# Performance work log

Measured on AMD Instinct MI355X. Metric: run time of the kernel, lower is better.

Reference implementation:

```python
import jax, jax.numpy as jnp
import numpy as np

B_, N_, D_ = 8, 1024, 64
H_, DH_ = 4, 16
DI_, DS_, DTR_ = 128, 64, 4
MAXP = 512


def _ln(x, w, b, eps=1e-5):
    m = jnp.mean(x, -1, keepdims=True)
    v = jnp.mean((x - m) ** 2, -1, keepdims=True)
    return (x - m) * jax.lax.rsqrt(v + eps) * w + b


def _attn(x, drop_mask, Wq, Wkv, Wo, bo, rel_emb):
    b, n, d = x.shape
    scale = DH_ ** -0.5
    q = (x @ Wq).reshape(b, n, H_, DH_).transpose(0, 2, 1, 3)
    kv = x @ Wkv
    k = kv[..., :d].reshape(b, n, H_, DH_).transpose(0, 2, 1, 3)
    v = kv[..., d:].reshape(b, n, H_, DH_).transpose(0, 2, 1, 3)
    dots = jnp.einsum('bhid,bhjd->bhij', q, k) * scale
    seq = jnp.arange(n)
    dist = jnp.clip(seq[:, None] - seq[None, :], -MAXP, MAXP) + MAXP
    rpe = rel_emb[dist]  # (n, n, DH_)
    dots = dots + jnp.einsum('bhid,ijd->bhij', q, rpe) * scale
    # stochastic key drop: Bernoulli(0.3) positions get -1e12
    dots = dots + drop_mask.astype(dots.dtype) * (-1e12)
    attn = jax.nn.softmax(dots, axis=-1)
    out = jnp.einsum('bhij,bhjd->bhid', attn, v)
    out = out.transpose(0, 2, 1, 3).reshape(b, n, H_ * DH_)
    return out @ Wo + bo


def _mamba(x, W_in, conv_w, conv_b, W_xproj, W_dt, b_dt, A_log, Dm, W_out):
    b, n, _ = x.shape
    xz = x @ W_in                      # (b, n, 2*DI_)
    u, z = xz[..., :DI_], xz[..., DI_:]
    uc = u.transpose(0, 2, 1)          # (b, DI_, n)
    uc = jax.lax.conv_general_dilated(
        uc, conv_w[:, None, :], (1,), ((3, 0),),
        feature_group_count=DI_, dimension_numbers=('NCH', 'OIH', 'NCH'))
    uc = uc + conv_b[None, :, None]
    u = jax.nn.silu(uc).transpose(0, 2, 1)  # (b, n, DI_)
    xdb = u @ W_xproj                  # (b, n, DTR_+2*DS_)
    dt = jax.nn.softplus(xdb[..., :DTR_] @ W_dt + b_dt)  # (b, n, DI_)
    Bm = xdb[..., DTR_:DTR_ + DS_]
    Cm = xdb[..., DTR_ + DS_:]
    A = -jnp.exp(A_log)                # (DI_, DS_)

    def step(h, inp):
        dt_t, B_t, C_t, u_t = inp      # (b,DI_),(b,DS_),(b,DS_),(b,DI_)
        dA = jnp.exp(dt_t[..., None] * A)
        h = h * dA + (dt_t * u_t)[..., None] * B_t[:, None, :]
        y = jnp.einsum('bds,bs->bd', h, C_t)
        return h, y

    h0 = jnp.zeros((b, DI_, DS_), x.dtype)
    xs = (dt.transpose(1, 0, 2), Bm.transpose(1, 0, 2),
          Cm.transpose(1, 0, 2), u.transpose(1, 0, 2))
    _, ys = jax.lax.scan(step, h0, xs)
    y = ys.transpose(1, 0, 2) + u * Dm
    y = y * jax.nn.silu(z)
    return y @ W_out


def _rmsgn(x, gamma, eps=1e-5, groups=4):
    shp = x.shape
    dpg = shp[-1] // groups
    xg = x.reshape(shp[:-1] + (groups, dpg))
    rms = jnp.sqrt(jnp.sum(xg * xg, -1, keepdims=True)) * (dpg ** -0.5)
    return (xg / (rms + eps)).reshape(shp) * gamma


def _ff1(x, c1_w, c1_b, d1_w, d1_b):
    # SwiGLUConvDeconv1d(64, 256, kernel=4, shift=1); x: (b, s2, 64)
    s2 = x.shape[1]
    xc = x.transpose(0, 2, 1)
    xc = jnp.pad(xc, ((0, 0), (0, 0), (3, 3)))
    xc = jax.lax.conv_general_dilated(
        xc, c1_w, (1,), 'VALID', dimension_numbers=('NCH', 'OIH', 'NCH'))
    xc = xc + c1_b[None, :, None]
    gate = jax.nn.silu(xc[:, 256:, :])
    xc = xc[:, :256, :] * gate
    # ConvTranspose1d stride 1 == conv with flipped kernel, full padding
    w = jnp.flip(d1_w, -1).transpose(1, 0, 2)  # (64, 256, 4)
    xc = jax.lax.conv_general_dilated(
        xc, w, (1,), ((3, 3),), dimension_numbers=('NCH', 'OIH', 'NCH'))
    xc = xc + d1_b[None, :, None]
    out = xc.transpose(0, 2, 1)
    return out[:, 3:3 + s2, :]


def _forward(x, drop_mask, ln1_w, ln1_b, Wq, Wkv, Wo, bo, rel_emb,
             ln2_w, ln2_b, W_in, conv_w, conv_b, W_xproj, W_dt, b_dt,
             A_log, Dm, W_out, gamma, c1_w, c1_b, d1_w, d1_b, ln3_w, ln3_b):
    xt = _ln(x, ln1_w, ln1_b)
    xt = _attn(xt, drop_mask, Wq, Wkv, Wo, bo, rel_emb) + x
    x = x + xt  # dropout p=0 -> identity (faithful to original residual math)
    xt = _ln(x, ln2_w, ln2_b)
    m = _mamba(xt, W_in, conv_w, conv_b, W_xproj, W_dt, b_dt, A_log, Dm, W_out)
    m = jnp.where(m >= 0, m, 0.01 * m)  # leaky_relu
    m = _rmsgn(m, gamma)
    m = m + 0.5 * _ff1(m, c1_w, c1_b, d1_w, d1_b)
    x = x + m
    return _ln(x, ln3_w, ln3_b)


def setup_inputs() -> dict:
    ks = jax.random.split(jax.random.key(0), 16)
    g = lambda i, shp, s: jax.random.normal(ks[i], shp, dtype=jnp.float32) * s
    A_log = jnp.log(jnp.tile(jnp.arange(1, DS_ + 1, dtype=jnp.float32)[None, :], (DI_, 1)))
    return {
        'x': jax.random.normal(ks[0], (B_, N_, D_), dtype=jnp.float32),
        'drop_mask': jax.random.bernoulli(ks[1], 0.3, (B_, H_, N_, N_)),
        'ln1_w': jnp.ones((D_,), jnp.float32), 'ln1_b': jnp.zeros((D_,), jnp.float32),
        'Wq': g(2, (D_, D_), 0.1), 'Wkv': g(3, (D_, 2 * D_), 0.1),
        'Wo': g(4, (D_, D_), 0.1), 'bo': jnp.zeros((D_,), jnp.float32),
        'rel_emb': g(5, (2 * MAXP + 1, DH_), 0.02),
        'ln2_w': jnp.ones((D_,), jnp.float32), 'ln2_b': jnp.zeros((D_,), jnp.float32),
        'W_in': g(6, (D_, 2 * DI_), 0.1),
        'conv_w': g(7, (DI_, 4), 0.2), 'conv_b': jnp.zeros((DI_,), jnp.float32),
        'W_xproj': g(8, (DI_, DTR_ + 2 * DS_), 0.1),
        'W_dt': g(9, (DTR_, DI_), 0.1), 'b_dt': jnp.zeros((DI_,), jnp.float32),
        'A_log': A_log, 'Dm': jnp.ones((DI_,), jnp.float32),
        'W_out': g(10, (DI_, D_), 0.1),
        'gamma': jnp.ones((D_,), jnp.float32),
        'c1_w': g(11, (512, 64, 4), 0.1), 'c1_b': jnp.zeros((512,), jnp.float32),
        'd1_w': g(12, (256, 64, 4), 0.1), 'd1_b': jnp.zeros((64,), jnp.float32),
        'ln3_w': jnp.ones((D_,), jnp.float32), 'ln3_b': jnp.zeros((D_,), jnp.float32),
    }


def reference(x, drop_mask, ln1_w, ln1_b, Wq, Wkv, Wo, bo, rel_emb,
              ln2_w, ln2_b, W_in, conv_w, conv_b, W_xproj, W_dt, b_dt,
              A_log, Dm, W_out, gamma, c1_w, c1_b, d1_w, d1_b, ln3_w, ln3_b):
    return _forward(x, drop_mask, ln1_w, ln1_b, Wq, Wkv, Wo, bo, rel_emb,
                    ln2_w, ln2_b, W_in, conv_w, conv_b, W_xproj, W_dt, b_dt,
                    A_log, Dm, W_out, gamma, c1_w, c1_b, d1_w, d1_b, ln3_w, ln3_b)
```

## Files before the change

### kernel.cpp

```cpp
#include <hip/hip_runtime.h>
#include <hip/hip_fp16.h>
#include <math.h>


__device__ __forceinline__ float wsum64(float v){
#pragma unroll
  for(int m=32;m>0;m>>=1) v += __shfl_xor(v, m, 64);
  return v;
}
__device__ __forceinline__ float wmax64(float v){
#pragma unroll
  for(int m=32;m>0;m>>=1) v = fmaxf(v, __shfl_xor(v, m, 64));
  return v;
}
__device__ __forceinline__ float silu_f(float x){ return x / (1.f + __expf(-x)); }
__device__ __forceinline__ float rfl_f(float x){
  return __int_as_float(__builtin_amdgcn_readfirstlane(__float_as_int(x)));
}

__global__ __launch_bounds__(256) void k_ln1_qkv(
    const float* __restrict__ x, const float* __restrict__ w1, const float* __restrict__ b1,
    const float* __restrict__ Wq, const float* __restrict__ Wkv,
    const float* __restrict__ rel, const float* __restrict__ c1w,
    const int* __restrict__ dmask,
    float* __restrict__ qb, float2* __restrict__ kvT,
    float* __restrict__ relT, float* __restrict__ c1wT,
    unsigned long long* __restrict__ mask64, unsigned* __restrict__ KmaxSq){
  int tid = threadIdx.x;
  int bi = blockIdx.x >> 1;
  if (blockIdx.x & 1){
    size_t base = (size_t)bi * 16384;
    const int4* dp4 = (const int4*)(dmask + base);
    unsigned long long* mp = mask64 + (base >> 6);
    int lane = tid & 63, wv = tid >> 6;
    int li = (lane & 15) * 4;
#pragma unroll 1
    for(int p=0; p<4; ++p){
      int4 v0 = dp4[p*1024 + tid*4 + 0];
      int4 v1 = dp4[p*1024 + tid*4 + 1];
      int4 v2 = dp4[p*1024 + tid*4 + 2];
      int4 v3 = dp4[p*1024 + tid*4 + 3];
      unsigned m = 0;
      m |= (v0.x!=0) ? 1u<<0  : 0u;  m |= (v0.y!=0) ? 1u<<1  : 0u;
      m |= (v0.z!=0) ? 1u<<2  : 0u;  m |= (v0.w!=0) ? 1u<<3  : 0u;
      m |= (v1.x!=0) ? 1u<<4  : 0u;  m |= (v1.y!=0) ? 1u<<5  : 0u;
      m |= (v1.z!=0) ? 1u<<6  : 0u;  m |= (v1.w!=0) ? 1u<<7  : 0u;
      m |= (v2.x!=0) ? 1u<<8  : 0u;  m |= (v2.y!=0) ? 1u<<9  : 0u;
      m |= (v2.z!=0) ? 1u<<10 : 0u;  m |= (v2.w!=0) ? 1u<<11 : 0u;
      m |= (v3.x!=0) ? 1u<<12 : 0u;  m |= (v3.y!=0) ? 1u<<13 : 0u;
      m |= (v3.z!=0) ? 1u<<14 : 0u;  m |= (v3.w!=0) ? 1u<<15 : 0u;
      unsigned s0 = __shfl(m, li+0, 64);
      unsigned s1 = __shfl(m, li+1, 64);
      unsigned s2 = __shfl(m, li+2, 64);
      unsigned s3 = __shfl(m, li+3, 64);
      if (lane < 16){
        unsigned long long word = (unsigned long long)s0
          | ((unsigned long long)s1 << 16)
          | ((unsigned long long)s2 << 32)
          | ((unsigned long long)s3 << 48);
        mp[p*64 + wv*16 + lane] = word;
      }
    }
    return;
  }
  int lane = tid & 63, warp = tid >> 6;
  int token = bi*4 + warp;
  __shared__ float xt[4][64];
  float xv = x[(size_t)token*64 + lane];
  float mean = wsum64(xv) * 0.015625f;
  float dlt = xv - mean;
  float var = wsum64(dlt*dlt) * 0.015625f;
  float xn = dlt * rsqrtf(var + 1e-5f) * w1[lane] + b1[lane];
  xt[warp][lane] = xn;
  __syncthreads();
  float aq=0.f, ak=0.f, av=0.f;
#pragma unroll 4
  for(int dd=0; dd<64; ++dd){
    float xd = xt[warp][dd];
    aq += xd * Wq[dd*64 + lane];
    ak += xd * Wkv[dd*128 + lane];
    av += xd * Wkv[dd*128 + 64 + lane];
  }
  int b = token >> 10, i = token & 1023;
  int h = lane >> 4, dh = lane & 15;
  size_t o  = (((size_t)(b*4 + h))*1024 + i)*16 + dh;
  size_t oT = (((size_t)(b*4 + h))*16 + dh)*1024 + i;
  qb[o]=aq;
  kvT[oT] = make_float2(ak, av);

  float kk = ak*ak;
  kk += __shfl_xor(kk, 1, 64);
  kk += __shfl_xor(kk, 2, 64);
  kk += __shfl_xor(kk, 4, 64);
  kk += __shfl_xor(kk, 8, 64);
  if (dh == 0) atomicMax(KmaxSq + (b*4 + h), __float_as_uint(kk));

  if (bi < 65){
    int idx = bi*256 + tid;
    if (idx < 16*1025){
      int c = idx / 1025;
      int d = idx - c*1025;
      relT[idx] = rel[d*16 + c];
    }
  } else if (bi < 577){
    int idx = (bi-65)*256 + tid;
    int row = idx >> 9;
    int ii  = idx & 511;
    c1wT[idx] = c1w[(size_t)ii*256 + row];
  }
}

__global__ __launch_bounds__(256, 2) void k_attn(
    const float* __restrict__ qb, const float2* __restrict__ kvT,
    const unsigned long long* __restrict__ mask64, const float* __restrict__ relT,
    const unsigned* __restrict__ KmaxSq, float* __restrict__ attn_raw){
  int tid = threadIdx.x;
  int lane = tid & 63;
  int wvu  = __builtin_amdgcn_readfirstlane(tid >> 6);
  int wg   = blockIdx.x;
  int xcd  = wg & 7;
  int slot = wg >> 3;
  int bh   = xcd*4 + (slot >> 6);
  int i0   = (slot & 63) * 16;
  int b = bh >> 2, h = bh & 3;
  int R0 = wvu*4, R1 = R0+1, R2 = R0+2, R3 = R0+3;

  __shared__ __align__(16) __half Gc[16][1040];
  __shared__ __align__(16) float4 kXV[2][64][9];
  __shared__ float qs[16][16];
  __shared__ float G0s[16], G1024s[16];
  __shared__ float gmS[16];
  __shared__ float Ms[16];
  __shared__ float sums[16];

  {
    int r = tid >> 4, c = tid & 15;
    qs[r][c] = qb[((size_t)bh*1024 + i0 + r)*16 + c] * 0.25f;
  }
  __syncthreads();

  float q0[16], q1[16], q2[16], q3[16];
#pragma unroll
  for(int c=0;c<16;++c){
    q0[c]=rfl_f(qs[R0][c]); q1[c]=rfl_f(qs[R1][c]);
    q2[c]=rfl_f(qs[R2][c]); q3[c]=rfl_f(qs[R3][c]);
  }

  const float2* kvb = kvT + (size_t)bh*16*1024;
  int jj = tid & 63, cg = tid >> 6;
  float2 st[4];
#define LOADREGS(CH) do{ int _j0=(CH)*64;                                   \
    _Pragma("unroll")                                                       \
    for(int i_=0;i_<4;++i_) st[i_]=kvb[(cg*4+i_)*1024 + _j0 + jj]; }while(0)
#define WRITEB(NB) do{                                                      \
    kXV[NB][jj][cg]  =make_float4(st[0].x,st[1].x,st[2].x,st[3].x);         \
    kXV[NB][jj][4+cg]=make_float4(st[0].y,st[1].y,st[2].y,st[3].y); }while(0)
#define LBAR() do{                                                          \
    asm volatile("s_waitcnt lgkmcnt(0)" ::: "memory");                      \
    __builtin_amdgcn_s_barrier();                                           \
    asm volatile("" ::: "memory"); }while(0)

  LOADREGS(0);

#pragma unroll 1
  for(int bb=0; bb<17; ++bb){
    int d = lane + 64*bb;
    if (d <= 1024){
      float rl[16];
#pragma unroll
      for(int c=0;c<16;++c) rl[c] = relT[c*1025 + d];
      float g0=0.f, g1=0.f, g2=0.f, g3=0.f;
#pragma unroll
      for(int c=0;c<16;++c){
        float rc = rl[c];
        g0 += q0[c]*rc; g1 += q1[c]*rc; g2 += q2[c]*rc; g3 += q3[c]*rc;
      }
      if (d == 0){ G0s[R0]=g0; G0s[R1]=g1; G0s[R2]=g2; G0s[R3]=g3; }
      else if (d == 1024){ G1024s[R0]=g0; G1024s[R1]=g1; G1024s[R2]=g2; G1024s[R3]=g3; }
      else {
        int j0r = i0 + 512 - d + R0;
        if (j0r+0 >= 0 && j0r+0 < 1024) Gc[R0][j0r+0] = __float2half_rn(g0);
        if (j0r+1 >= 0 && j0r+1 < 1024) Gc[R1][j0r+1] = __float2half_rn(g1);
        if (j0r+2 >= 0 && j0r+2 < 1024) Gc[R2][j0r+2] = __float2half_rn(g2);
        if (j0r+3 >= 0 && j0r+3 < 1024) Gc[R3][j0r+3] = __float2half_rn(g3);
      }
    }
  }
  __syncthreads();
  {
    const unsigned long long* mrow = mask64 + ((size_t)bh*1024 + i0)*16;
#pragma unroll 1
    for(int r=0;r<16;++r){
      float g0 = G0s[r], g1 = G1024s[r];
      int lo = i0 + r - 512;
      int hi = i0 + r + 512;
#pragma unroll
      for(int p=0;p<4;++p){
        int j = tid + 256*p;
        unsigned long long w = mrow[r*16 + (j>>6)];
        float g;
        if (j >= hi) g = g0;
        else if (j <= lo) g = g1;
        else g = __half2float(Gc[r][j]);
        if ((w >> (j & 63)) & 1ULL) g = -60000.f;
        Gc[r][j] = __float2half_rn(g);
      }
    }
  }
  __syncthreads();
  {
    int r = tid >> 4, l4 = tid & 15;
    float gm = -3.0e38f;
#pragma unroll
    for(int k=0;k<64;++k) gm = fmaxf(gm, __half2float(Gc[r][l4 + 16*k]));
#pragma unroll
    for(int m=1;m<16;m<<=1) gm = fmaxf(gm, __shfl_xor(gm, m, 64));
    if (l4 == 0) gmS[r] = gm;
  }
  __syncthreads();
  if (tid < 16){
    float qn = 0.f;
#pragma unroll
    for(int c=0;c<16;++c) qn += qs[tid][c]*qs[tid][c];
    float km = sqrtf(__uint_as_float(KmaxSq[bh]));
    Ms[tid] = gmS[tid] + sqrtf(qn)*km;
  }
  __syncthreads();

  float M0 = rfl_f(Ms[R0]), M1 = rfl_f(Ms[R1]);
  float M2 = rfl_f(Ms[R2]), M3 = rfl_f(Ms[R3]);

  float s0=0.f, s1=0.f, s2=0.f, s3=0.f;
  float a0[16], a1[16], a2[16], a3[16];
#pragma unroll
  for(int c=0;c<16;++c){ a0[c]=0.f; a1[c]=0.f; a2[c]=0.f; a3[c]=0.f; }

  WRITEB(0);
  LOADREGS(1);
  LBAR();
  int cur = 0;

#pragma unroll 1
  for(int ch=0; ch<16; ++ch){
    int j = ch*64 + lane;
    float sv0 = __half2float(Gc[R0][j]), sv1 = __half2float(Gc[R1][j]);
    float sv2 = __half2float(Gc[R2][j]), sv3 = __half2float(Gc[R3][j]);
#pragma unroll
    for(int c4=0;c4<4;++c4){
      float4 kx = kXV[cur][lane][c4];
      sv0 += q0[4*c4+0]*kx.x + q0[4*c4+1]*kx.y + q0[4*c4+2]*kx.z + q0[4*c4+3]*kx.w;
      sv1 += q1[4*c4+0]*kx.x + q1[4*c4+1]*kx.y + q1[4*c4+2]*kx.z + q1[4*c4+3]*kx.w;
      sv2 += q2[4*c4+0]*kx.x + q2[4*c4+1]*kx.y + q2[4*c4+2]*kx.z + q2[4*c4+3]*kx.w;
      sv3 += q3[4*c4+0]*kx.x + q3[4*c4+1]*kx.y + q3[4*c4+2]*kx.z + q3[4*c4+3]*kx.w;
    }
    float p0 = __expf(sv0 - M0), p1 = __expf(sv1 - M1);
    float p2 = __expf(sv2 - M2), p3 = __expf(sv3 - M3);
    s0 += p0; s1 += p1; s2 += p2; s3 += p3;
#pragma unroll
    for(int c4=0;c4<4;++c4){
      float4 vy = kXV[cur][lane][4+c4];
      a0[4*c4+0] += p0*vy.x; a0[4*c4+1] += p0*vy.y; a0[4*c4+2] += p0*vy.z; a0[4*c4+3] += p0*vy.w;
      a1[4*c4+0] += p1*vy.x; a1[4*c4+1] += p1*vy.y; a1[4*c4+2] += p1*vy.z; a1[4*c4+3] += p1*vy.w;
      a2[4*c4+0] += p2*vy.x; a2[4*c4+1] += p2*vy.y; a2[4*c4+2] += p2*vy.z; a2[4*c4+3] += p2*vy.w;
      a3[4*c4+0] += p3*vy.x; a3[4*c4+1] += p3*vy.y; a3[4*c4+2] += p3*vy.z; a3[4*c4+3] += p3*vy.w;
    }
    if (ch < 15){
      WRITEB(cur^1);
      if (ch < 14) LOADREGS(ch+2);
    }
    LBAR();
    cur ^= 1;
  }
#undef LOADREGS
#undef WRITEB
#undef LBAR

  s0 = wsum64(s0); s1 = wsum64(s1); s2 = wsum64(s2); s3 = wsum64(s3);
#pragma unroll
  for(int c=0;c<16;++c){
    float x0 = a0[c]; x0 += __shfl_xor(x0,32,64); x0 += __shfl_xor(x0,16,64); a0[c] = x0;
    float x1 = a1[c]; x1 += __shfl_xor(x1,32,64); x1 += __shfl_xor(x1,16,64); a1[c] = x1;
    float x2 = a2[c]; x2 += __shfl_xor(x2,32,64); x2 += __shfl_xor(x2,16,64); a2[c] = x2;
    float x3 = a3[c]; x3 += __shfl_xor(x3,32,64); x3 += __shfl_xor(x3,16,64); a3[c] = x3;
  }
  __syncthreads();
  float* red = (float*)&Gc[0][0];
  if (lane < 16){
#pragma unroll
    for(int c=0;c<16;++c){
      red[R0*272 + lane*17 + c] = a0[c];
      red[R1*272 + lane*17 + c] = a1[c];
      red[R2*272 + lane*17 + c] = a2[c];
      red[R3*272 + lane*17 + c] = a3[c];
    }
  }
  if (lane == 0){ sums[R0]=s0; sums[R1]=s1; sums[R2]=s2; sums[R3]=s3; }
  __syncthreads();
  {
    int row = tid >> 4, c = tid & 15;
    float tot = 0.f;
#pragma unroll
    for(int g=0; g<16; ++g) tot += red[row*272 + g*17 + c];
    attn_raw[((size_t)b*1024 + i0 + row)*64 + h*16 + c] = tot / sums[row];
  }
}

__global__ __launch_bounds__(256) void k_post_attn(
    const float* __restrict__ x, const float* __restrict__ attn_raw,
    const float* __restrict__ Wo, const float* __restrict__ bo,
    const float* __restrict__ ln2w, const float* __restrict__ ln2b,
    const float* __restrict__ W_in,
    float* __restrict__ x2, float* __restrict__ u0, float* __restrict__ zsarr){
  int tid = threadIdx.x;
  int lane = tid & 63, wv = tid >> 6;
  int tok0 = blockIdx.x * 16;
  __shared__ float arS[16][64];
  __shared__ float lnS[16][64];
  for(int l = tid; l < 1024; l += 256)
    arS[l >> 6][l & 63] = attn_raw[(size_t)tok0*64 + l];
  __syncthreads();
#pragma unroll 1
  for(int tt = 0; tt < 4; ++tt){
    int tl = wv*4 + tt;
    int token = tok0 + tl;
    float acc = bo[lane];
#pragma unroll 4
    for(int dd = 0; dd < 64; ++dd) acc += arS[tl][dd] * Wo[dd*64 + lane];
    float t = 2.f*x[(size_t)token*64 + lane] + acc;
    x2[(size_t)token*64 + lane] = t;
    float mean = wsum64(t)*0.015625f;
    float dlt = t - mean;
    float var = wsum64(dlt*dlt)*0.015625f;
    lnS[tl][lane] = dlt*rsqrtf(var+1e-5f)*ln2w[lane] + ln2b[lane];
  }
  __syncthreads();
  int oc = tid;
  float w[64];
#pragma unroll
  for(int dd = 0; dd < 64; ++dd) w[dd] = W_in[dd*256 + oc];
  const float4* lnS4 = (const float4*)&lnS[0][0];
#pragma unroll 1
  for(int tl = 0; tl < 16; ++tl){
    float acc = 0.f;
#pragma unroll
    for(int d4 = 0; d4 < 16; ++d4){
      float4 l4 = lnS4[tl*16 + d4];
      acc += l4.x*w[4*d4] + l4.y*w[4*d4+1] + l4.z*w[4*d4+2] + l4.w*w[4*d4+3];
    }
    int token = tok0 + tl;
    if (oc < 128) u0[(size_t)token*128 + oc] = acc;
    else          zsarr[(size_t)token*128 + (oc-128)] = silu_f(acc);
  }
}

__global__ __launch_bounds__(256) void k_conv_proj(
    const float* __restrict__ u0, const float* __restrict__ conv_w, const float* __restrict__ conv_b,
    const float* __restrict__ W_xproj, const float* __restrict__ W_dt, const float* __restrict__ b_dt,
    float* __restrict__ uarr, float* __restrict__ Bmp, float* __restrict__ Cmp, float* __restrict__ dtarr){
  int sub = threadIdx.x >> 7, c = threadIdx.x & 127;
  int token = blockIdx.x*2 + sub;
  int b = token >> 10, i = token & 1023;
  __shared__ float us[2][128];
  __shared__ float dtin[2][4];
  float acc = conv_b[c];
#pragma unroll
  for(int k2=0;k2<4;++k2){
    int t2 = i - 3 + k2;
    if (t2 >= 0) acc += u0[((size_t)b*1024 + t2)*128 + c]*conv_w[c*4+k2];
  }
  float uv = silu_f(acc);
  uarr[(size_t)token*128 + c] = uv;
  us[sub][c] = uv;
  __syncthreads();
  float accA = 0.f, accB = 0.f;
  int cB = 128 + (c & 3);
#pragma unroll 4
  for(int dd=0; dd<128; ++dd){
    float xd = us[sub][dd];
    accA += xd * W_xproj[dd*132 + c];
    accB += xd * W_xproj[dd*132 + cB];
  }
  if (c < 4){ dtin[sub][c] = accA; Cmp[(size_t)token*64 + 60 + c] = accB; }
  else if (c < 68) Bmp[(size_t)token*64 + (c-4)] = accA;
  else             Cmp[(size_t)token*64 + (c-68)] = accA;
  __syncthreads();
  float dv = b_dt[c];
#pragma unroll
  for(int r2=0;r2<4;++r2) dv += dtin[sub][r2]*W_dt[r2*128 + c];
  dv = fmaxf(dv, 0.f) + log1pf(expf(-fabsf(dv)));
  dtarr[(size_t)token*128 + c] = dv;
}

__global__ __launch_bounds__(512) void k_scan(
    const float* __restrict__ dtarr, const float* __restrict__ uarr,
    const float* __restrict__ Bmp, const float* __restrict__ Cmp,
    const float* __restrict__ zsarr, const float* __restrict__ A_log,
    const float* __restrict__ Dm, float* __restrict__ ymp){
  int lane = threadIdx.x & 63, c = threadIdx.x >> 6;
  int wg = blockIdx.x;
  int b = wg & 7;
  int d = wg >> 3;
  __shared__ float Ps[8][64], Rs[8][64];
  float A = -expf(A_log[d*64 + lane]);
  float Dv = Dm[d];
  int tb = c*128;
  const float* dtp = dtarr + ((size_t)b*1024 + tb)*128 + d;
  const float* up  = uarr  + ((size_t)b*1024 + tb)*128 + d;
  const float* zp  = zsarr + ((size_t)b*1024 + tb)*128 + d;
  const float* Bp  = Bmp   + ((size_t)b*1024 + tb)*64 + lane;
  const float* Cp  = Cmp   + ((size_t)b*1024 + tb)*64 + lane;
  float* yp        = ymp   + ((size_t)b*1024 + tb)*128 + d;
  float R = 0.f, sdt = 0.f;
  for(int t0=0; t0<128; t0+=8){
    float dtc[8], uc[8], Bc[8];
#pragma unroll
    for(int r=0;r<8;++r){
      dtc[r]=dtp[(size_t)(t0+r)*128]; uc[r]=up[(size_t)(t0+r)*128]; Bc[r]=Bp[(size_t)(t0+r)*64];
    }
#pragma unroll
    for(int r=0;r<8;++r){
      float dt = dtc[r];
      R = R*__expf(dt*A) + dt*uc[r]*Bc[r];
      sdt += dt;
    }
  }
  Ps[c][lane] = __expf(sdt*A);
  Rs[c][lane] = R;
  __syncthreads();
  float h = 0.f;
#pragma unroll 1
  for(int cp=0; cp<c; ++cp) h = h*Ps[cp][lane] + Rs[cp][lane];
  for(int t0=0; t0<128; t0+=8){
    float dtc[8], uc[8], Bc[8], Cc[8], zc[8];
#pragma unroll
    for(int r=0;r<8;++r){
      dtc[r]=dtp[(size_t)(t0+r)*128]; uc[r]=up[(size_t)(t0+r)*128];
      Bc[r]=Bp[(size_t)(t0+r)*64];    Cc[r]=Cp[(size_t)(t0+r)*64];
      zc[r]=zp[(size_t)(t0+r)*128];
    }
    float hc[8];
#pragma unroll
    for(int r=0;r<8;++r){
      float dt = dtc[r];
      h = h*__expf(dt*A) + dt*uc[r]*Bc[r];
      hc[r] = h*Cc[r];
    }
    float y[8];
#pragma unroll
    for(int r=0;r<8;++r) y[r] = wsum64(hc[r]);
    if (lane==0){
#pragma unroll
      for(int r=0;r<8;++r) yp[(size_t)(t0+r)*128] = (y[r] + uc[r]*Dv)*zc[r];
    }
  }
}

__global__ __launch_bounds__(256) void k_wout(
    const float* __restrict__ ymp, const float* __restrict__ W_out,
    const float* __restrict__ gamma, float* __restrict__ marr){
  int lane = threadIdx.x & 63, warp = threadIdx.x >> 6;
  int token = blockIdx.x*4 + warp;
  __shared__ float ys[4][128];
  ys[warp][lane]      = ymp[(size_t)token*128 + lane];
  ys[warp][lane+64]   = ymp[(size_t)token*128 + 64 + lane];
  __syncthreads();
  float acc = 0.f;
#pragma unroll 4
  for(int dd=0; dd<128; ++dd) acc += ys[warp][dd]*W_out[dd*64 + lane];
  acc = acc >= 0.f ? acc : 0.01f*acc;
  float ss = acc*acc;
#pragma unroll
  for(int m=1;m<16;m<<=1) ss += __shfl_xor(ss, m, 64);
  float rms = sqrtf(ss)*0.25f;
  marr[(size_t)token*64 + lane] = acc/(rms + 1e-5f)*gamma[lane];
}

__global__ __launch_bounds__(256) void k_h2(
    const float* __restrict__ marr, const float* __restrict__ c1wT,
    const float* __restrict__ c1b, float* __restrict__ h2){
  int b = blockIdx.y;
  int t0 = blockIdx.x * 16;
  int tid = threadIdx.x;
  __shared__ float ms[19][64];
  for(int l = tid; l < 19*64; l += 256){
    int row = l >> 6, cc = l & 63;
    int t = t0 - 3 + row;
    ms[row][cc] = (t >= 0 && t < 1024) ? marr[((size_t)b*1024 + t)*64 + cc] : 0.f;
  }
  __syncthreads();
  int i = tid;
  float acc1[16], acc2[16];
#pragma unroll
  for(int tl=0;tl<16;++tl){ acc1[tl]=0.f; acc2[tl]=0.f; }
  for(int cc=0; cc<64; ++cc){
    float mv[19];
#pragma unroll
    for(int r2=0;r2<19;++r2) mv[r2] = ms[r2][cc];
    const float* wr = c1wT + (size_t)cc*4*512;
    float wa0 = wr[      i], wa1 = wr[ 512+i], wa2 = wr[1024+i], wa3 = wr[1536+i];
    float wg0 = wr[  256+i], wg1 = wr[ 768+i], wg2 = wr[1280+i], wg3 = wr[1792+i];
#pragma unroll
    for(int tl=0; tl<16; ++tl){
      acc1[tl] += wa0*mv[tl+0] + wa1*mv[tl+1] + wa2*mv[tl+2] + wa3*mv[tl+3];
      acc2[tl] += wg0*mv[tl+0] + wg1*mv[tl+1] + wg2*mv[tl+2] + wg3*mv[tl+3];
    }
  }
  float bb1 = c1b[i], bb2 = c1b[i+256];
#pragma unroll
  for(int tl=0; tl<16; ++tl){
    int t = t0 + tl;
    if (t < 1027){
      float o1 = acc1[tl] + bb1;
      float o2 = acc2[tl] + bb2;
      h2[((size_t)b*1027 + t)*256 + i] = o1 * silu_f(o2);
    }
  }
}

__global__ __launch_bounds__(256) void k_ff_final(
    const float* __restrict__ h2, const float* __restrict__ d1w, const float* __restrict__ d1b,
    const float* __restrict__ x2, const float* __restrict__ marr,
    const float* __restrict__ ln3w, const float* __restrict__ ln3b,
    float* __restrict__ out){
  int b = blockIdx.y;
  int s0 = blockIdx.x * 16;
  int tid = threadIdx.x;
  int o = tid & 63, sg = tid >> 6;
  __shared__ float hs[19][256];
  for(int l = tid; l < 19*256; l += 256){
    int row = l >> 8, cc = l & 255;
    hs[row][cc] = h2[((size_t)b*1027 + s0 + row)*256 + cc];
  }
  __syncthreads();
  int sl = sg*4;
  float acc0=0.f, acc1=0.f, acc2=0.f, acc3=0.f;
  const float4* wb = (const float4*)d1w + o;
#pragma unroll 2
  for(int i2=0; i2<256; ++i2){
    float4 wv = wb[(size_t)i2*64];
    float h0=hs[sl+0][i2], h1=hs[sl+1][i2], h2v=hs[sl+2][i2], h3=hs[sl+3][i2];
    float h4=hs[sl+4][i2], h5=hs[sl+5][i2], h6=hs[sl+6][i2];
    acc0 += h0*wv.w + h1*wv.z + h2v*wv.y + h3*wv.x;
    acc1 += h1*wv.w + h2v*wv.z + h3*wv.y + h4*wv.x;
    acc2 += h2v*wv.w + h3*wv.z + h4*wv.y + h5*wv.x;
    acc3 += h3*wv.w + h4*wv.z + h5*wv.y + h6*wv.x;
  }
  float accs[4] = {acc0, acc1, acc2, acc3};
  float bo_ = d1b[o];
#pragma unroll
  for(int r=0;r<4;++r){
    int s = s0 + sl + r;
    size_t idx = ((size_t)b*1024 + s)*64 + o;
    float tot = x2[idx] + marr[idx] + 0.5f*(accs[r] + bo_);
    float mean = wsum64(tot)*0.015625f;
    float dlt = tot - mean;
    float var = wsum64(dlt*dlt)*0.015625f;
    out[idx] = dlt*rsqrtf(var+1e-5f)*ln3w[o] + ln3b[o];
  }
}

extern "C" void kernel_launch(void* const* d_in, const int* in_sizes, int n_in,
                              void* d_out, int out_size, void* d_ws, size_t ws_size,
                              hipStream_t stream){
  const float* x       = (const float*)d_in[0];
  const int*   dmask   = (const int*)  d_in[1];
  const float* ln1w    = (const float*)d_in[2];
  const float* ln1b    = (const float*)d_in[3];
  const float* Wq      = (const float*)d_in[4];
  const float* Wkv     = (const float*)d_in[5];
  const float* Wo      = (const float*)d_in[6];
  const float* bo      = (const float*)d_in[7];
  const float* rel     = (const float*)d_in[8];
  const float* ln2w    = (const float*)d_in[9];
  const float* ln2b    = (const float*)d_in[10];
  const float* W_in    = (const float*)d_in[11];
  const float* conv_w  = (const float*)d_in[12];
  const float* conv_b  = (const float*)d_in[13];
  const float* W_xproj = (const float*)d_in[14];
  const float* W_dt    = (const float*)d_in[15];
  const float* b_dt    = (const float*)d_in[16];
  const float* A_log   = (const float*)d_in[17];
  const float* Dm      = (const float*)d_in[18];
  const float* W_out   = (const float*)d_in[19];
  const float* gamma   = (const float*)d_in[20];
  const float* c1w     = (const float*)d_in[21];
  const float* c1b     = (const float*)d_in[22];
  const float* d1w     = (const float*)d_in[23];
  const float* d1b     = (const float*)d_in[24];
  const float* ln3w    = (const float*)d_in[25];
  const float* ln3b    = (const float*)d_in[26];
  float* outp = (float*)d_out;

  float* ws = (float*)d_ws;
  float* qb       = ws;
  float* kvT      = qb      + 524288;
  float* attn_raw = kvT     + 1048576;
  float* x2       = attn_raw+ 524288;
  float* u0       = x2      + 524288;
  float* zsarr    = u0      + 1048576;
  float* uarr     = zsarr   + 1048576;
  float* dtarr    = uarr    + 1048576;
  float* Bmp      = dtarr   + 1048576;
  float* Cmp      = Bmp     + 524288;
  float* ymp      = Cmp     + 524288;
  float* marr     = ymp     + 1048576;
  float* h2       = marr    + 524288;
  float* relT     = h2      + 2103296;
  float* c1wT     = relT    + 16400;
  float* Parr     = c1wT    + 131072;
  float* Rarr     = Parr    + 524288;
  float* Kmaxa    = Rarr    + 524288;

  unsigned long long* mask64 = (unsigned long long*)h2;
  unsigned* KmaxSqU = (unsigned*)Kmaxa;

  hipMemsetAsync(KmaxSqU, 0, 32*sizeof(unsigned), stream);
  k_ln1_qkv  <<<4096, 256, 0, stream>>>(x, ln1w, ln1b, Wq, Wkv, rel, c1w, dmask,
                                        qb, (float2*)kvT, relT, c1wT, mask64, KmaxSqU);
  k_attn     <<<2048, 256, 0, stream>>>(qb, (const float2*)kvT, mask64, relT, KmaxSqU, attn_raw);
  k_post_attn<<<512, 256, 0, stream>>>(x, attn_raw, Wo, bo, ln2w, ln2b, W_in, x2, u0, zsarr);
  k_conv_proj<<<4096, 256, 0, stream>>>(u0, conv_w, conv_b, W_xproj, W_dt, b_dt, uarr, Bmp, Cmp, dtarr);
  k_scan     <<<1024, 512, 0, stream>>>(dtarr, uarr, Bmp, Cmp, zsarr, A_log, Dm, ymp);
  k_wout     <<<2048, 256, 0, stream>>>(ymp, W_out, gamma, marr);
  k_h2       <<<dim3(65,8), 256, 0, stream>>>(marr, c1wT, c1b, h2);
  k_ff_final <<<dim3(64,8), 256, 0, stream>>>(h2, d1w, d1b, x2, marr, ln3w, ln3b, outp);
}
```

Measured before the change: 691.9 us.

## Fuse conv/projection into post-attention kernel and W_out into h2 kernel

Merges the depthwise conv, x-projection and dt computation into the post-attention kernel. The 3-token causal halo is handled by recomputing the Wo/LN2/W_in path for three extra rows per 16-token block. Separately, the W_out projection, leaky-ReLU and RMS-norm step moves into the h2 kernel, which recomputes it for its halo rows from ymp. This removes two launches and the u0 and marr global round-trips on the read side, at the cost of redundant halo compute and more shared memory and serial work per block.

```diff
diff --git a/kernel.cpp b/kernel.cpp
--- a/kernel.cpp
+++ b/kernel.cpp
@@ -310,85 +310,106 @@
     const float* __restrict__ Wo, const float* __restrict__ bo,
     const float* __restrict__ ln2w, const float* __restrict__ ln2b,
     const float* __restrict__ W_in,
-    float* __restrict__ x2, float* __restrict__ u0, float* __restrict__ zsarr){
+    const float* __restrict__ conv_w, const float* __restrict__ conv_b,
+    const float* __restrict__ W_xproj, const float* __restrict__ W_dt,
+    const float* __restrict__ b_dt,
+    float* __restrict__ x2, float* __restrict__ zsarr,
+    float* __restrict__ uarr, float* __restrict__ Bmp,
+    float* __restrict__ Cmp, float* __restrict__ dtarr){
   int tid = threadIdx.x;
   int lane = tid & 63, wv = tid >> 6;
   int tok0 = blockIdx.x * 16;
-  __shared__ float arS[16][64];
-  __shared__ float lnS[16][64];
-  for(int l = tid; l < 1024; l += 256)
-    arS[l >> 6][l & 63] = attn_raw[(size_t)tok0*64 + l];
-  __syncthreads();
-#pragma unroll 1
-  for(int tt = 0; tt < 4; ++tt){
-    int tl = wv*4 + tt;
+  bool halo_ok = ((tok0 & 1023) != 0);
+  __shared__ float arS[19][64];
+  __shared__ float lnS[19][64];
+  __shared__ float u0S[19][128];
+  __shared__ float usS[16][128];
+  __shared__ float dtinS[16][4];
+  for(int l = tid; l < 19*64; l += 256){
+    int row = l >> 6, cc = l & 63;
+    int token = tok0 - 3 + row;
+    arS[row][cc] = (row >= 3 || halo_ok) ? attn_raw[(size_t)token*64 + cc] : 0.f;
+  }
+  __syncthreads();
+#pragma unroll 1
+  for(int tt = 0; tt < 5; ++tt){
+    int tl = wv + 4*tt;
+    if (tl < 19){
+      int token = tok0 - 3 + tl;
+      if (tl >= 3 || halo_ok){
+        float acc = bo[lane];
+#pragma unroll 4
+        for(int dd = 0; dd < 64; ++dd) acc += arS[tl][dd] * Wo[dd*64 + lane];
+        float t = 2.f*x[(size_t)token*64 + lane] + acc;
+        if (tl >= 3) x2[(size_t)token*64 + lane] = t;
+        float mean = wsum64(t)*0.015625f;
+        float dlt = t - mean;
+        float var = wsum64(dlt*dlt)*0.015625f;
+        lnS[tl][lane] = dlt*rsqrtf(var+1e-5f)*ln2w[lane] + ln2b[lane];
+      } else {
+        lnS[tl][lane] = 0.f;
+      }
+    }
+  }
+  __syncthreads();
+  {
+    int oc = tid;
+    float w[64];
+#pragma unroll
+    for(int dd = 0; dd < 64; ++dd) w[dd] = W_in[dd*256 + oc];
+    const float4* lnS4 = (const float4*)&lnS[0][0];
+#pragma unroll 1
+    for(int tl = 0; tl < 19; ++tl){
+      float acc = 0.f;
+#pragma unroll
+      for(int d4 = 0; d4 < 16; ++d4){
+        float4 l4 = lnS4[tl*16 + d4];
+        acc += l4.x*w[4*d4] + l4.y*w[4*d4+1] + l4.z*w[4*d4+2] + l4.w*w[4*d4+3];
+      }
+      if (oc < 128) u0S[tl][oc] = acc;
+      else if (tl >= 3) zsarr[(size_t)(tok0 + tl - 3)*128 + (oc-128)] = silu_f(acc);
+    }
+  }
+  __syncthreads();
+  int sub = tid >> 7, c = tid & 127;
+#pragma unroll 1
+  for(int pr = 0; pr < 8; ++pr){
+    int tl = pr*2 + sub;
+    float acc = conv_b[c];
+#pragma unroll
+    for(int k2 = 0; k2 < 4; ++k2)
+      acc += u0S[tl + k2][c] * conv_w[c*4 + k2];
+    float uv = silu_f(acc);
+    uarr[(size_t)(tok0 + tl)*128 + c] = uv;
+    usS[tl][c] = uv;
+  }
+  __syncthreads();
+#pragma unroll 1
+  for(int pr = 0; pr < 8; ++pr){
+    int tl = pr*2 + sub;
     int token = tok0 + tl;
-    float acc = bo[lane];
+    float accA = 0.f, accB = 0.f;
+    int cB = 128 + (c & 3);
 #pragma unroll 4
-    for(int dd = 0; dd < 64; ++dd) acc += arS[tl][dd] * Wo[dd*64 + lane];
-    float t = 2.f*x[(size_t)token*64 + lane] + acc;
-    x2[(size_t)token*64 + lane] = t;
-    float mean = wsum64(t)*0.015625f;
-    float dlt = t - mean;
-    float var = wsum64(dlt*dlt)*0.015625f;
-    lnS[tl][lane] = dlt*rsqrtf(var+1e-5f)*ln2w[lane] + ln2b[lane];
-  }
-  __syncthreads();
-  int oc = tid;
-  float w[64];
-#pragma unroll
-  for(int dd = 0; dd < 64; ++dd) w[dd] = W_in[dd*256 + oc];
-  const float4* lnS4 = (const float4*)&lnS[0][0];
-#pragma unroll 1
-  for(int tl = 0; tl < 16; ++tl){
-    float acc = 0.f;
-#pragma unroll
-    for(int d4 = 0; d4 < 16; ++d4){
-      float4 l4 = lnS4[tl*16 + d4];
-      acc += l4.x*w[4*d4] + l4.y*w[4*d4+1] + l4.z*w[4*d4+2] + l4.w*w[4*d4+3];
-    }
-    int token = tok0 + tl;
-    if (oc < 128) u0[(size_t)token*128 + oc] = acc;
-    else          zsarr[(size_t)token*128 + (oc-128)] = silu_f(acc);
-  }
-}
-
-__global__ __launch_bounds__(256) void k_conv_proj(
-    const float* __restrict__ u0, const float* __restrict__ conv_w, const float* __restrict__ conv_b,
-    const float* __restrict__ W_xproj, const float* __restrict__ W_dt, const float* __restrict__ b_dt,
-    float* __restrict__ uarr, float* __restrict__ Bmp, float* __restrict__ Cmp, float* __restrict__ dtarr){
-  int sub = threadIdx.x >> 7, c = threadIdx.x & 127;
-  int token = blockIdx.x*2 + sub;
-  int b = token >> 10, i = token & 1023;
-  __shared__ float us[2][128];
-  __shared__ float dtin[2][4];
-  float acc = conv_b[c];
-#pragma unroll
-  for(int k2=0;k2<4;++k2){
-    int t2 = i - 3 + k2;
-    if (t2 >= 0) acc += u0[((size_t)b*1024 + t2)*128 + c]*conv_w[c*4+k2];
-  }
-  float uv = silu_f(acc);
-  uarr[(size_t)token*128 + c] = uv;
-  us[sub][c] = uv;
-  __syncthreads();
-  float accA = 0.f, accB = 0.f;
-  int cB = 128 + (c & 3);
-#pragma unroll 4
-  for(int dd=0; dd<128; ++dd){
-    float xd = us[sub][dd];
-    accA += xd * W_xproj[dd*132 + c];
-    accB += xd * W_xproj[dd*132 + cB];
-  }
-  if (c < 4){ dtin[sub][c] = accA; Cmp[(size_t)token*64 + 60 + c] = accB; }
-  else if (c < 68) Bmp[(size_t)token*64 + (c-4)] = accA;
-  else             Cmp[(size_t)token*64 + (c-68)] = accA;
-  __syncthreads();
-  float dv = b_dt[c];
-#pragma unroll
-  for(int r2=0;r2<4;++r2) dv += dtin[sub][r2]*W_dt[r2*128 + c];
-  dv = fmaxf(dv, 0.f) + log1pf(expf(-fabsf(dv)));
-  dtarr[(size_t)token*128 + c] = dv;
+    for(int dd = 0; dd < 128; ++dd){
+      float xd = usS[tl][dd];
+      accA += xd * W_xproj[dd*132 + c];
+      accB += xd * W_xproj[dd*132 + cB];
+    }
+    if (c < 4){ dtinS[tl][c] = accA; Cmp[(size_t)token*64 + 60 + c] = accB; }
+    else if (c < 68) Bmp[(size_t)token*64 + (c-4)] = accA;
+    else             Cmp[(size_t)token*64 + (c-68)] = accA;
+  }
+  __syncthreads();
+#pragma unroll 1
+  for(int pr = 0; pr < 8; ++pr){
+    int tl = pr*2 + sub;
+    float dv = b_dt[c];
+#pragma unroll
+    for(int r2 = 0; r2 < 4; ++r2) dv += dtinS[tl][r2]*W_dt[r2*128 + c];
+    dv = fmaxf(dv, 0.f) + log1pf(expf(-fabsf(dv)));
+    dtarr[(size_t)(tok0 + tl)*128 + c] = dv;
+  }
 }
 
 __global__ __launch_bounds__(512) void k_scan(
@@ -455,37 +476,42 @@
   }
 }
 
-__global__ __launch_bounds__(256) void k_wout(
+__global__ __launch_bounds__(256) void k_h2(
     const float* __restrict__ ymp, const float* __restrict__ W_out,
-    const float* __restrict__ gamma, float* __restrict__ marr){
-  int lane = threadIdx.x & 63, warp = threadIdx.x >> 6;
-  int token = blockIdx.x*4 + warp;
-  __shared__ float ys[4][128];
-  ys[warp][lane]      = ymp[(size_t)token*128 + lane];
-  ys[warp][lane+64]   = ymp[(size_t)token*128 + 64 + lane];
-  __syncthreads();
-  float acc = 0.f;
-#pragma unroll 4
-  for(int dd=0; dd<128; ++dd) acc += ys[warp][dd]*W_out[dd*64 + lane];
-  acc = acc >= 0.f ? acc : 0.01f*acc;
-  float ss = acc*acc;
-#pragma unroll
-  for(int m=1;m<16;m<<=1) ss += __shfl_xor(ss, m, 64);
-  float rms = sqrtf(ss)*0.25f;
-  marr[(size_t)token*64 + lane] = acc/(rms + 1e-5f)*gamma[lane];
-}
-
-__global__ __launch_bounds__(256) void k_h2(
-    const float* __restrict__ marr, const float* __restrict__ c1wT,
-    const float* __restrict__ c1b, float* __restrict__ h2){
+    const float* __restrict__ gamma,
+    const float* __restrict__ c1wT, const float* __restrict__ c1b,
+    float* __restrict__ marr, float* __restrict__ h2){
   int b = blockIdx.y;
   int t0 = blockIdx.x * 16;
   int tid = threadIdx.x;
+  __shared__ float ys[19][128];
   __shared__ float ms[19][64];
-  for(int l = tid; l < 19*64; l += 256){
-    int row = l >> 6, cc = l & 63;
+  for(int l = tid; l < 19*128; l += 256){
+    int row = l >> 7, cc = l & 127;
     int t = t0 - 3 + row;
-    ms[row][cc] = (t >= 0 && t < 1024) ? marr[((size_t)b*1024 + t)*64 + cc] : 0.f;
+    ys[row][cc] = (t >= 0 && t < 1024) ? ymp[((size_t)b*1024 + t)*128 + cc] : 0.f;
+  }
+  __syncthreads();
+  {
+    int o = tid & 63, wvi = tid >> 6;
+#pragma unroll 1
+    for(int bt = 0; bt < 5; ++bt){
+      int row = bt*4 + wvi;
+      if (row < 19){
+        float acc = 0.f;
+#pragma unroll 4
+        for(int dd = 0; dd < 128; ++dd) acc += ys[row][dd]*W_out[dd*64 + o];
+        acc = acc >= 0.f ? acc : 0.01f*acc;
+        float ss = acc*acc;
+#pragma unroll
+        for(int m=1;m<16;m<<=1) ss += __shfl_xor(ss, m, 64);
+        float rms = sqrtf(ss)*0.25f;
+        float mv = acc/(rms + 1e-5f)*gamma[o];
+        ms[row][o] = mv;
+        int t = t0 - 3 + row;
+        if (row >= 3 && t < 1024) marr[((size_t)b*1024 + t)*64 + o] = mv;
+      }
+    }
   }
   __syncthreads();
   int i = tid;
@@ -618,10 +644,10 @@
   k_ln1_qkv  <<<4096, 256, 0, stream>>>(x, ln1w, ln1b, Wq, Wkv, rel, c1w, dmask,
                                         qb, (float2*)kvT, relT, c1wT, mask64, KmaxSqU);
   k_attn     <<<2048, 256, 0, stream>>>(qb, (const float2*)kvT, mask64, relT, KmaxSqU, attn_raw);
-  k_post_attn<<<512, 256, 0, stream>>>(x, attn_raw, Wo, bo, ln2w, ln2b, W_in, x2, u0, zsarr);
-  k_conv_proj<<<4096, 256, 0, stream>>>(u0, conv_w, conv_b, W_xproj, W_dt, b_dt, uarr, Bmp, Cmp, dtarr);
+  k_post_attn<<<512, 256, 0, stream>>>(x, attn_raw, Wo, bo, ln2w, ln2b, W_in,
+                                       conv_w, conv_b, W_xproj, W_dt, b_dt,
+                                       x2, zsarr, uarr, Bmp, Cmp, dtarr);
   k_scan     <<<1024, 512, 0, stream>>>(dtarr, uarr, Bmp, Cmp, zsarr, A_log, Dm, ymp);
-  k_wout     <<<2048, 256, 0, stream>>>(ymp, W_out, gamma, marr);
-  k_h2       <<<dim3(65,8), 256, 0, stream>>>(marr, c1wT, c1b, h2);
+  k_h2       <<<dim3(65,8), 256, 0, stream>>>(ymp, W_out, gamma, c1wT, c1b, marr, h2);
   k_ff_final <<<dim3(64,8), 256, 0, stream>>>(h2, d1w, d1b, x2, marr, ln3w, ln3b, outp);
 }
```

Result: slower. 715.2 us (+3.4%).
